# Performance work log

Measured on AMD Instinct MI355X. Metric: run time of the kernel, lower is better.

## Reference

```python
import jax, jax.numpy as jnp
import numpy as np

K = 7          # involution kernel size
G = 16         # groups = channels // group_channels = 256 // 16
BN_EPS = 1e-3  # Keras BatchNormalization default epsilon


def setup_inputs() -> dict:
    key = jax.random.key(0)
    ks = jax.random.split(key, 6)
    B, H, W, C = 4, 56, 56, 256
    Cr = C // 4                      # reduction_ratio = 4
    x = jax.random.normal(ks[0], (B, H, W, C), dtype=jnp.float32)
    w_reduce = jax.random.normal(ks[1], (C, Cr), dtype=jnp.float32) * (1.0 / np.sqrt(C))
    gamma = jnp.ones((Cr,), dtype=jnp.float32)
    beta = jnp.zeros((Cr,), dtype=jnp.float32)
    mean = jax.random.normal(ks[2], (Cr,), dtype=jnp.float32) * 0.1
    var = jax.random.uniform(ks[3], (Cr,), dtype=jnp.float32) + 0.5
    w_span = jax.random.normal(ks[4], (Cr, K * K * G), dtype=jnp.float32) * (1.0 / np.sqrt(Cr))
    b_span = jnp.zeros((K * K * G,), dtype=jnp.float32)
    return {"x": x, "w_reduce": w_reduce, "gamma": gamma, "beta": beta,
            "mean": mean, "var": var, "w_span": w_span, "b_span": b_span}


def reference(x, w_reduce, gamma, beta, mean, var, w_span, b_span):
    B, H, W, C = x.shape
    Cg = C // G  # channels per group
    # kernel generation branch: 1x1 conv -> BN (inference) -> ReLU -> 1x1 conv
    r = jnp.einsum('bhwc,cd->bhwd', x, w_reduce)
    r = jax.nn.relu((r - mean) * (gamma / jnp.sqrt(var + BN_EPS)) + beta)
    kgen = jnp.einsum('bhwd,de->bhwe', r, w_span) + b_span      # (B,H,W,K*K*G)
    kgen = kgen.reshape(B, H, W, G, K * K)
    # im2col with SAME padding (stride=1, pad (K-1)//2 symmetric), depth order (kh, kw, C)
    p = (K - 1) // 2
    xp = jnp.pad(x, ((0, 0), (p, p), (p, p), (0, 0)))
    patches = jnp.stack([xp[:, i:i + H, j:j + W, :]
                         for i in range(K) for j in range(K)], axis=3)  # (B,H,W,K*K,C)
    patches = patches.reshape(B, H, W, K * K, G, Cg)
    # per-pixel, per-group weighted reduction over the K*K window
    out = jnp.einsum('bhwgk,bhwkgc->bhwgc', kgen, patches)
    return out.reshape(B, H, W, C)
```

## Files before the change

### kernel.cpp

```cpp
#include <hip/hip_runtime.h>
#include <hip/hip_bf16.h>
#include <stdint.h>

#define B_   4
#define H_   56
#define W_   56
#define C_   256
#define CR   64
#define G_   16
#define CG   16
#define KS   7
#define KK   49
#define PADR 3
#define NPX  (B_*H_*W_)

typedef __attribute__((ext_vector_type(8))) short bf16x8;
typedef __attribute__((ext_vector_type(4))) float f32x4;
typedef __attribute__((ext_vector_type(2))) float f32x2;

__device__ __forceinline__ uint32_t f2bf(float f) {
    uint32_t x = __float_as_uint(f);
    return (x + 0x7fffu + ((x >> 16) & 1u)) >> 16;
}
__device__ __forceinline__ uint32_t pkbf(float a, float b) {
    union { __hip_bfloat162 h; uint32_t u; } c;
    c.h = __float22bfloat162_rn(make_float2(a, b));
    return c.u;
}
__device__ __forceinline__ float blo(uint32_t w) { return __uint_as_float(w << 16); }
__device__ __forceinline__ float bhi(uint32_t w) { return __uint_as_float(w & 0xffff0000u); }

union U4V { uint4 u; bf16x8 v; };

__global__ __launch_bounds__(256) void k0_prepack(
        const float* __restrict__ wr, const float* __restrict__ wspan,
        const float* __restrict__ gamma, const float* __restrict__ beta,
        const float* __restrict__ mean, const float* __restrict__ var,
        uint16_t* __restrict__ wrp, uint16_t* __restrict__ wpp,
        float* __restrict__ scale, float* __restrict__ shift) {
    int idx = blockIdx.x * 256 + threadIdx.x;
    {
        int j = idx & 7, lane = (idx >> 3) & 63, nb = (idx >> 9) & 3,
            kb = (idx >> 11) & 1, g = idx >> 12;
        int k = kb * 32 + (lane >> 4) * 8 + j;
        int n = nb * 16 + (lane & 15);
        float v = (n < KK) ? wspan[k * (KK * G_) + g * KK + n] : 0.f;
        wpp[idx] = (uint16_t)f2bf(v);
    }
    if (idx < 16384) {
        int j = idx & 7, lane = (idx >> 3) & 63, nb = (idx >> 9) & 3, kb = idx >> 11;
        int k = kb * 32 + (lane >> 4) * 8 + j;
        int n = nb * 16 + (lane & 15);
        wrp[idx] = (uint16_t)f2bf(wr[k * CR + n]);
    }
    if (idx < CR) {
        float s = gamma[idx] * rsqrtf(var[idx] + 1e-3f);
        scale[idx] = s;
        shift[idx] = beta[idx] - mean[idx] * s;
    }
}

__global__ __launch_bounds__(256) void k1_reduce(
        const float* __restrict__ x, const uint16_t* __restrict__ wrp,
        const float* __restrict__ scale, const float* __restrict__ shift,
        uint16_t* __restrict__ r, uint16_t* __restrict__ xbf) {
    int tid = threadIdx.x;
    int lane = tid & 63, w = tid >> 6;
    int mt = blockIdx.x * 4 + w;
    int pix = mt * 16 + (lane & 15);
    int ko = (lane >> 4) * 8;
    const float* xrow = x + (size_t)pix * C_ + ko;
    f32x4 acc[4] = {{0,0,0,0},{0,0,0,0},{0,0,0,0},{0,0,0,0}};
    for (int kb = 0; kb < 8; ++kb) {
        float4 a0 = *(const float4*)(xrow + kb * 32);
        float4 a1 = *(const float4*)(xrow + kb * 32 + 4);
        U4V af;
        af.u = make_uint4(pkbf(a0.x, a0.y), pkbf(a0.z, a0.w),
                          pkbf(a1.x, a1.y), pkbf(a1.z, a1.w));
        *(uint4*)(xbf + (size_t)pix * C_ + ko + kb * 32) = af.u;
        const uint16_t* wb = wrp + kb * 2048 + lane * 8;
        #pragma unroll
        for (int nb = 0; nb < 4; ++nb) {
            bf16x8 bf_ = *(const bf16x8*)(wb + nb * 512);
            acc[nb] = __builtin_amdgcn_mfma_f32_16x16x32_bf16(af.v, bf_, acc[nb], 0, 0, 0);
        }
    }
    int rq = (lane >> 4) * 4;
    #pragma unroll
    for (int nb = 0; nb < 4; ++nb) {
        int d = nb * 16 + (lane & 15);
        float s = scale[d], sh = shift[d];
        #pragma unroll
        for (int rg = 0; rg < 4; ++rg) {
            float v = fmaf(acc[nb][rg], s, sh);
            v = v > 0.f ? v : 0.f;
            r[(size_t)(mt * 16 + rq + rg) * CR + d] = (uint16_t)f2bf(v);
        }
    }
}

#define TS   14
#define HS   20
#define XSW  16
#define KGW  56

__global__ __launch_bounds__(256, 4) void k2_involution(
        const uint16_t* __restrict__ xbf, const uint16_t* __restrict__ r,
        const uint16_t* __restrict__ wpp, const float* __restrict__ bspan,
        float* __restrict__ out) {
    __shared__ __align__(16) uint16_t xs[HS * HS * XSW];
    __shared__ __align__(16) uint16_t kg[196 * KGW];

    int tid  = threadIdx.x;
    int tile = blockIdx.x, g = blockIdx.y, b = blockIdx.z;
    int ty0 = (tile >> 2) * TS, tx0 = (tile & 3) * TS;

    #pragma unroll
    for (int pass = 0; pass < 2; ++pass) {
        int i = tid + pass * 256;
        if (i < HS * HS) {
            int py = i / HS, px = i % HS;
            int gy = ty0 + py - PADR, gx = tx0 + px - PADR;
            uint4 wA = make_uint4(0, 0, 0, 0), wB = wA;
            if (gy >= 0 && gy < H_ && gx >= 0 && gx < W_) {
                const uint16_t* xp = xbf + (((size_t)(b * H_ + gy)) * W_ + gx) * C_ + g * CG;
                wA = *(const uint4*)(xp);
                wB = *(const uint4*)(xp + 8);
            }
            uint16_t* dst = xs + i * XSW;
            *(uint4*)(dst + 0) = wA;
            *(uint4*)(dst + 8) = wB;
        }
    }

    int lane = tid & 63, w = tid >> 6;
    bf16x8 bfr[2][4];
    const uint16_t* wb = wpp + g * 4096 + lane * 8;
    #pragma unroll
    for (int kb = 0; kb < 2; ++kb)
        #pragma unroll
        for (int nb = 0; nb < 4; ++nb)
            bfr[kb][nb] = *(const bf16x8*)(wb + kb * 2048 + nb * 512);
    float bias[4];
    #pragma unroll
    for (int nb = 0; nb < 4; ++nb) {
        int n = nb * 16 + (lane & 15);
        bias[nb] = (n < KK) ? bspan[g * KK + n] : 0.f;
    }
    for (int mi = 0; mi < 4; ++mi) {
        int mt = mi * 4 + w;
        if (mt < 13) {
            int m  = mt * 16 + (lane & 15);
            int mm = m < 196 ? m : 195;
            int ly = mm / TS, lx = mm % TS;
            size_t pix = ((size_t)(b * H_ + ty0 + ly)) * W_ + (tx0 + lx);
            const uint16_t* rp = r + pix * CR + (lane >> 4) * 8;
            bf16x8 a0 = *(const bf16x8*)(rp);
            bf16x8 a1 = *(const bf16x8*)(rp + 32);
            f32x4 acc[4];
            #pragma unroll
            for (int nb = 0; nb < 4; ++nb)
                acc[nb] = (f32x4){bias[nb], bias[nb], bias[nb], bias[nb]};
            #pragma unroll
            for (int nb = 0; nb < 4; ++nb) {
                acc[nb] = __builtin_amdgcn_mfma_f32_16x16x32_bf16(a0, bfr[0][nb], acc[nb], 0, 0, 0);
                acc[nb] = __builtin_amdgcn_mfma_f32_16x16x32_bf16(a1, bfr[1][nb], acc[nb], 0, 0, 0);
            }
            int row = mt * 16 + (lane >> 4) * 4;
            if (row < 196) {
                #pragma unroll
                for (int nb = 0; nb < 4; ++nb) {
                    int n = nb * 16 + (lane & 15);
                    if (n < KK) {
                        int slot = n + n / 7;
                        #pragma unroll
                        for (int rg = 0; rg < 4; ++rg)
                            kg[(row + rg) * KGW + slot] = (uint16_t)f2bf(acc[nb][rg]);
                    }
                }
            }
        }
    }
    __syncthreads();

    if (tid < 196) {
        int p = tid >> 1, h = tid & 1;
        int ty = p / 7, tx = (p % 7) * 2;
        const uint16_t* kgL = kg + (ty * TS + tx) * KGW;
        const uint16_t* kgR = kgL + KGW;

        f32x2 accL[4] = {{0,0},{0,0},{0,0},{0,0}};
        f32x2 accR[4] = {{0,0},{0,0},{0,0},{0,0}};
        #pragma unroll
        for (int kh = 0; kh < KS; ++kh) {
            uint4 aL = *(const uint4*)(kgL + kh * 8);
            uint4 aR = *(const uint4*)(kgR + kh * 8);
            const uint32_t kwL[4] = {aL.x, aL.y, aL.z, aL.w};
            const uint32_t kwR[4] = {aR.x, aR.y, aR.z, aR.w};
            const uint16_t* xrow = xs + ((ty + kh) * HS + tx) * XSW + h * 8;
            #pragma unroll
            for (int j = 0; j < 8; ++j) {
                uint4 xw = *(const uint4*)(xrow + j * XSW);
                float kvL = 0.f, kvR = 0.f;
                if (j < 7) kvL = (j & 1) ? bhi(kwL[j >> 1]) : blo(kwL[j >> 1]);
                if (j > 0) { int t = j - 1; kvR = (t & 1) ? bhi(kwR[t >> 1]) : blo(kwR[t >> 1]); }
                f32x2 kL = {kvL, kvL}, kR = {kvR, kvR};
                f32x2 x0 = {blo(xw.x), bhi(xw.x)};
                f32x2 x1 = {blo(xw.y), bhi(xw.y)};
                f32x2 x2 = {blo(xw.z), bhi(xw.z)};
                f32x2 x3 = {blo(xw.w), bhi(xw.w)};
                accL[0] = __builtin_elementwise_fma(kL, x0, accL[0]);
                accL[1] = __builtin_elementwise_fma(kL, x1, accL[1]);
                accL[2] = __builtin_elementwise_fma(kL, x2, accL[2]);
                accL[3] = __builtin_elementwise_fma(kL, x3, accL[3]);
                accR[0] = __builtin_elementwise_fma(kR, x0, accR[0]);
                accR[1] = __builtin_elementwise_fma(kR, x1, accR[1]);
                accR[2] = __builtin_elementwise_fma(kR, x2, accR[2]);
                accR[3] = __builtin_elementwise_fma(kR, x3, accR[3]);
            }
        }
        size_t pixL = ((size_t)(b * H_ + ty0 + ty)) * W_ + (tx0 + tx);
        float* opL = out + pixL * C_ + g * CG + h * 8;
        float* opR = opL + C_;
        *(float4*)(opL + 0) = make_float4(accL[0].x, accL[0].y, accL[1].x, accL[1].y);
        *(float4*)(opL + 4) = make_float4(accL[2].x, accL[2].y, accL[3].x, accL[3].y);
        *(float4*)(opR + 0) = make_float4(accR[0].x, accR[0].y, accR[1].x, accR[1].y);
        *(float4*)(opR + 4) = make_float4(accR[2].x, accR[2].y, accR[3].x, accR[3].y);
    }
}

extern "C" void kernel_launch(void* const* d_in, const int* in_sizes, int n_in,
                              void* d_out, int out_size, void* d_ws, size_t ws_size,
                              hipStream_t stream) {
    const float* x        = (const float*)d_in[0];
    const float* w_reduce = (const float*)d_in[1];
    const float* gamma    = (const float*)d_in[2];
    const float* beta     = (const float*)d_in[3];
    const float* mean     = (const float*)d_in[4];
    const float* var      = (const float*)d_in[5];
    const float* w_span   = (const float*)d_in[6];
    const float* b_span   = (const float*)d_in[7];
    float* out = (float*)d_out;

    uint8_t* ws = (uint8_t*)d_ws;
    uint16_t* r_ws  = (uint16_t*)(ws + 0);
    uint16_t* wrp   = (uint16_t*)(ws + 1605632);
    uint16_t* wpp   = (uint16_t*)(ws + 1638400);
    float*    scale = (float*)   (ws + 1769472);
    float*    shift = (float*)   (ws + 1769728);
    uint16_t* xbf   = (uint16_t*)(ws + 1769984);

    hipLaunchKernelGGL(k0_prepack, dim3(256), dim3(256), 0, stream,
                       w_reduce, w_span, gamma, beta, mean, var,
                       wrp, wpp, scale, shift);
    hipLaunchKernelGGL(k1_reduce, dim3(NPX / 64), dim3(256), 0, stream,
                       x, wrp, scale, shift, r_ws, xbf);
    hipLaunchKernelGGL(k2_involution, dim3(16, 16, B_), dim3(256), 0, stream,
                       xbf, r_ws, wpp, b_span, out);
}
```

Baseline: 99.07 us.

## Fuse weight prepacking into reduce and involution kernels, drop prepack launch

Removes the separate prepack kernel. Each k1 block now converts w_reduce to bf16 into shared memory itself, and BN scale/shift are computed inline. k2 builds its w_span MFMA fragments directly from fp32 global memory with strided loads. This saves one kernel launch and its dependency, but every block now repeats the weight conversion, adding 32KB of LDS in k1 and uncoalesced strided loads in k2.

```diff
diff --git a/kernel.cpp b/kernel.cpp
--- a/kernel.cpp
+++ b/kernel.cpp
@@ -32,40 +32,29 @@
 
 union U4V { uint4 u; bf16x8 v; };
 
-__global__ __launch_bounds__(256) void k0_prepack(
-        const float* __restrict__ wr, const float* __restrict__ wspan,
+__global__ __launch_bounds__(256) void k1_reduce(
+        const float* __restrict__ x, const float* __restrict__ wr,
         const float* __restrict__ gamma, const float* __restrict__ beta,
         const float* __restrict__ mean, const float* __restrict__ var,
-        uint16_t* __restrict__ wrp, uint16_t* __restrict__ wpp,
-        float* __restrict__ scale, float* __restrict__ shift) {
-    int idx = blockIdx.x * 256 + threadIdx.x;
-    {
-        int j = idx & 7, lane = (idx >> 3) & 63, nb = (idx >> 9) & 3,
-            kb = (idx >> 11) & 1, g = idx >> 12;
-        int k = kb * 32 + (lane >> 4) * 8 + j;
-        int n = nb * 16 + (lane & 15);
-        float v = (n < KK) ? wspan[k * (KK * G_) + g * KK + n] : 0.f;
-        wpp[idx] = (uint16_t)f2bf(v);
-    }
-    if (idx < 16384) {
-        int j = idx & 7, lane = (idx >> 3) & 63, nb = (idx >> 9) & 3, kb = idx >> 11;
-        int k = kb * 32 + (lane >> 4) * 8 + j;
-        int n = nb * 16 + (lane & 15);
-        wrp[idx] = (uint16_t)f2bf(wr[k * CR + n]);
-    }
-    if (idx < CR) {
-        float s = gamma[idx] * rsqrtf(var[idx] + 1e-3f);
-        scale[idx] = s;
-        shift[idx] = beta[idx] - mean[idx] * s;
-    }
-}
-
-__global__ __launch_bounds__(256) void k1_reduce(
-        const float* __restrict__ x, const uint16_t* __restrict__ wrp,
-        const float* __restrict__ scale, const float* __restrict__ shift,
         uint16_t* __restrict__ r, uint16_t* __restrict__ xbf) {
+    __shared__ __align__(16) uint16_t wrl[16384];
     int tid = threadIdx.x;
     int lane = tid & 63, w = tid >> 6;
+
+    #pragma unroll
+    for (int s = 0; s < 8; ++s) {
+        int run = tid + s * 256;
+        int rl = run & 63, nb = (run >> 6) & 3, kb = run >> 8;
+        int n = nb * 16 + (rl & 15);
+        int kbase = kb * 32 + (rl >> 4) * 8;
+        uint32_t pk0 = pkbf(wr[(kbase + 0) * CR + n], wr[(kbase + 1) * CR + n]);
+        uint32_t pk1 = pkbf(wr[(kbase + 2) * CR + n], wr[(kbase + 3) * CR + n]);
+        uint32_t pk2 = pkbf(wr[(kbase + 4) * CR + n], wr[(kbase + 5) * CR + n]);
+        uint32_t pk3 = pkbf(wr[(kbase + 6) * CR + n], wr[(kbase + 7) * CR + n]);
+        *(uint4*)(wrl + run * 8) = make_uint4(pk0, pk1, pk2, pk3);
+    }
+    __syncthreads();
+
     int mt = blockIdx.x * 4 + w;
     int pix = mt * 16 + (lane & 15);
     int ko = (lane >> 4) * 8;
@@ -78,7 +67,7 @@
         af.u = make_uint4(pkbf(a0.x, a0.y), pkbf(a0.z, a0.w),
                           pkbf(a1.x, a1.y), pkbf(a1.z, a1.w));
         *(uint4*)(xbf + (size_t)pix * C_ + ko + kb * 32) = af.u;
-        const uint16_t* wb = wrp + kb * 2048 + lane * 8;
+        const uint16_t* wb = wrl + kb * 2048 + lane * 8;
         #pragma unroll
         for (int nb = 0; nb < 4; ++nb) {
             bf16x8 bf_ = *(const bf16x8*)(wb + nb * 512);
@@ -89,7 +78,8 @@
     #pragma unroll
     for (int nb = 0; nb < 4; ++nb) {
         int d = nb * 16 + (lane & 15);
-        float s = scale[d], sh = shift[d];
+        float s  = gamma[d] * rsqrtf(var[d] + 1e-3f);
+        float sh = beta[d] - mean[d] * s;
         #pragma unroll
         for (int rg = 0; rg < 4; ++rg) {
             float v = fmaf(acc[nb][rg], s, sh);
@@ -106,7 +96,7 @@
 
 __global__ __launch_bounds__(256, 4) void k2_involution(
         const uint16_t* __restrict__ xbf, const uint16_t* __restrict__ r,
-        const uint16_t* __restrict__ wpp, const float* __restrict__ bspan,
+        const float* __restrict__ wspan, const float* __restrict__ bspan,
         float* __restrict__ out) {
     __shared__ __align__(16) uint16_t xs[HS * HS * XSW];
     __shared__ __align__(16) uint16_t kg[196 * KGW];
@@ -135,18 +125,33 @@
 
     int lane = tid & 63, w = tid >> 6;
     bf16x8 bfr[2][4];
-    const uint16_t* wb = wpp + g * 4096 + lane * 8;
-    #pragma unroll
-    for (int kb = 0; kb < 2; ++kb)
-        #pragma unroll
-        for (int nb = 0; nb < 4; ++nb)
-            bfr[kb][nb] = *(const bf16x8*)(wb + kb * 2048 + nb * 512);
+    #pragma unroll
+    for (int kb = 0; kb < 2; ++kb) {
+        #pragma unroll
+        for (int nb = 0; nb < 4; ++nb) {
+            int n = nb * 16 + (lane & 15);
+            int kbase = kb * 32 + (lane >> 4) * 8;
+            U4V u;
+            if (n < KK) {
+                const float* wp = wspan + g * KK + n;
+                u.u = make_uint4(
+                    pkbf(wp[(size_t)(kbase + 0) * (KK * G_)], wp[(size_t)(kbase + 1) * (KK * G_)]),
+                    pkbf(wp[(size_t)(kbase + 2) * (KK * G_)], wp[(size_t)(kbase + 3) * (KK * G_)]),
+                    pkbf(wp[(size_t)(kbase + 4) * (KK * G_)], wp[(size_t)(kbase + 5) * (KK * G_)]),
+                    pkbf(wp[(size_t)(kbase + 6) * (KK * G_)], wp[(size_t)(kbase + 7) * (KK * G_)]));
+            } else {
+                u.u = make_uint4(0, 0, 0, 0);
+            }
+            bfr[kb][nb] = u.v;
+        }
+    }
     float bias[4];
     #pragma unroll
     for (int nb = 0; nb < 4; ++nb) {
         int n = nb * 16 + (lane & 15);
         bias[nb] = (n < KK) ? bspan[g * KK + n] : 0.f;
     }
+
     for (int mi = 0; mi < 4; ++mi) {
         int mt = mi * 4 + w;
         if (mt < 13) {
@@ -243,18 +248,11 @@
     float* out = (float*)d_out;
 
     uint8_t* ws = (uint8_t*)d_ws;
-    uint16_t* r_ws  = (uint16_t*)(ws + 0);
-    uint16_t* wrp   = (uint16_t*)(ws + 1605632);
-    uint16_t* wpp   = (uint16_t*)(ws + 1638400);
-    float*    scale = (float*)   (ws + 1769472);
-    float*    shift = (float*)   (ws + 1769728);
-    uint16_t* xbf   = (uint16_t*)(ws + 1769984);
-
-    hipLaunchKernelGGL(k0_prepack, dim3(256), dim3(256), 0, stream,
-                       w_reduce, w_span, gamma, beta, mean, var,
-                       wrp, wpp, scale, shift);
+    uint16_t* r_ws = (uint16_t*)(ws + 0);
+    uint16_t* xbf  = (uint16_t*)(ws + 1605632);
+
     hipLaunchKernelGGL(k1_reduce, dim3(NPX / 64), dim3(256), 0, stream,
-                       x, wrp, scale, shift, r_ws, xbf);
+                       x, w_reduce, gamma, beta, mean, var, r_ws, xbf);
     hipLaunchKernelGGL(k2_involution, dim3(16, 16, B_), dim3(256), 0, stream,
-                       xbf, r_ws, wpp, b_span, out);
-}
+                       xbf, r_ws, w_span, b_span, out);
+}
```

Result: no change. 100.2 us (+1.2%).
